# Kernel optimization log

Measured on AMD Instinct MI355X. Metric: run time of the kernel, lower is better.

Reference implementation:

```python
import jax, jax.numpy as jnp
import numpy as np

HIDDEN = 256
ATOM_DIM = 133
BOND_DIM = 14
MOL_DIM = 200
N_ATOMS = 120000
N_BONDS = 240000
MAX_DEG = 6
N_MOL = 4096
DEPTH = 3
EPS = 1e-5
NEG_SLOPE = 0.01


def _leaky(x):
    return jnp.where(x >= 0, x, NEG_SLOPE * x)


def _bn(x, w, b):
    # BatchNorm1d in training mode: batch mean / biased batch variance
    mu = jnp.mean(x, axis=0)
    var = jnp.var(x, axis=0)
    return (x - mu) * jax.lax.rsqrt(var + EPS) * w + b


def setup_inputs() -> dict:
    key = jax.random.key(0)
    ks = jax.random.split(key, 12)
    s = 0.02
    return {
        "atom_features": jax.random.normal(ks[0], (N_ATOMS, ATOM_DIM), jnp.float32),
        "bond_features": jax.random.normal(ks[1], (N_BONDS, BOND_DIM), jnp.float32),
        "bond_index": jax.random.randint(ks[2], (2, N_BONDS), 0, N_ATOMS, jnp.int32),
        "molecule_features": jax.random.normal(ks[3], (N_MOL, MOL_DIM), jnp.float32),
        # 1-based bond ids; 0 means padding (maps to prepended zero row)
        "atom_incoming_bond_map": jax.random.randint(ks[4], (N_ATOMS, MAX_DEG), 0, N_BONDS + 1, jnp.int32),
        "bond_reverse_map": jax.random.randint(ks[5], (N_BONDS,), 0, N_BONDS, jnp.int32),
        "atom_to_mol": jnp.sort(jax.random.randint(ks[6], (N_ATOMS,), 0, N_MOL, jnp.int32)),
        "W_i_w": jax.random.normal(ks[7], (HIDDEN, ATOM_DIM + BOND_DIM), jnp.float32) * s,
        "W_i_b": jnp.zeros((HIDDEN,), jnp.float32),
        "W_m_w": jax.random.normal(ks[8], (HIDDEN, HIDDEN), jnp.float32) * s,
        "W_m_b": jnp.zeros((HIDDEN,), jnp.float32),
        "W_a_w": jax.random.normal(ks[9], (HIDDEN, ATOM_DIM + HIDDEN), jnp.float32) * s,
        "W_a_b": jnp.zeros((HIDDEN,), jnp.float32),
        "bn_w": jnp.ones((HIDDEN,), jnp.float32),
        "bn_b": jnp.zeros((HIDDEN,), jnp.float32),
    }


def _atom_incoming_sum(h, aibm):
    # padded_h[0] is the zero row; aibm holds 1-based bond indices (0 = pad)
    padded_h = jnp.concatenate([jnp.zeros((1, h.shape[1]), h.dtype), h], axis=0)
    return padded_h[aibm].sum(axis=1)  # [n_atoms, H]


def reference(atom_features, bond_features, bond_index, molecule_features,
              atom_incoming_bond_map, bond_reverse_map, atom_to_mol,
              W_i_w, W_i_b, W_m_w, W_m_b, W_a_w, W_a_b, bn_w, bn_b):
    src = bond_index[0]
    # initial bond hidden states
    x = jnp.concatenate([bond_features, atom_features[src]], axis=1)
    h0 = _bn(_leaky(x @ W_i_w.T + W_i_b), bn_w, bn_b)
    h = h0
    for _ in range(DEPTH):
        atom_sums = _atom_incoming_sum(h, atom_incoming_bond_map)
        # message for bond b (v->w): sum of incoming bonds at v minus reverse bond
        m = atom_sums[src] - h[bond_reverse_map]
        h = _bn(_leaky(h0 + m @ W_m_w.T + W_m_b), bn_w, bn_b)
        # dropout_prob = 0.0 -> identity
    # bond -> atom pooling (empty atoms yield the cached zero vector)
    m_v = _atom_incoming_sum(h, atom_incoming_bond_map)
    h_v = _bn(_leaky(jnp.concatenate([atom_features, m_v], axis=1) @ W_a_w.T + W_a_b), bn_w, bn_b)
    # atom -> molecule pooling
    h_mol = jax.ops.segment_sum(h_v, atom_to_mol, num_segments=molecule_features.shape[0])
    return jnp.concatenate([h_mol, molecule_features], axis=1)
```

## Files before the change

### kernel.cpp

```cpp
#include <hip/hip_runtime.h>
#include <hip/hip_bf16.h>
#include <stdint.h>

#define NBONDS 240000
#define NATOMS 120000
#define HID    256
#define ADIM   133
#define BDIM   14
#define MOLDIM 200
#define NMOL   4096
#define KI     160
#define KM     256
#define KA     416
#define OUTW   456
#define BN_EPS 1e-5f
#define SLOPE  0.01f

typedef unsigned short u16;
typedef unsigned int   u32;
typedef __attribute__((ext_vector_type(8))) short short8;
typedef __attribute__((ext_vector_type(4))) float f32x4;

__device__ __forceinline__ float bf2f(u16 b){
  u32 u = ((u32)b) << 16;
  return __builtin_bit_cast(float, u);
}
__device__ __forceinline__ u16 f2bf(float f){
  u32 u = __builtin_bit_cast(u32, f);
  u32 r = (u + 0x7FFFu + ((u >> 16) & 1u)) >> 16;
  return (u16)r;
}
__device__ __forceinline__ void gload16(const void* g, void* l){
  __builtin_amdgcn_global_load_lds((const __attribute__((address_space(1))) u32*)g,
                                   (__attribute__((address_space(3))) u32*)l, 16, 0, 0);
}
__device__ __forceinline__ float leaky(float v){ return v >= 0.f ? v : SLOPE*v; }

__global__ void zero_f(float* p, int n){
  int i = blockIdx.x*blockDim.x + threadIdx.x;
  if(i < n) p[i] = 0.f;
}
__global__ void diag_k(float* out, int n, float wsz){
  int i = blockIdx.x*blockDim.x + threadIdx.x;
  for(; i < n; i += gridDim.x*blockDim.x) out[i] = (i == 0) ? wsz : 0.f;
}

__global__ void cvt_weights(const float* wi, const float* wm, const float* wa,
                            u16* wib, u16* wmb, u16* wab){
  int idx = blockIdx.x*blockDim.x + threadIdx.x;
  const int T0 = 256*KI, T1 = T0 + 256*KM, T2 = T1 + 256*KA;
  for(; idx < T2; idx += gridDim.x*blockDim.x){
    if(idx < T0){
      int n = idx / KI, k = idx % KI;
      float v = 0.f;
      if(k < 133)      v = wi[n*147 + 14 + k];
      else if(k < 147) v = wi[n*147 + (k - 133)];
      wib[idx] = f2bf(v);
    } else if(idx < T1){
      int j = idx - T0;
      wmb[j] = f2bf(wm[j]);
    } else {
      int j = idx - T1;
      int n = j / KA, k = j % KA;
      float v = 0.f;
      if(k < 256)      v = wa[n*389 + 133 + k];
      else if(k < 389) v = wa[n*389 + (k - 256)];
      wab[j] = f2bf(v);
    }
  }
}

__global__ void affine_k(const float* __restrict__ stats, float* __restrict__ aff,
                         float invN, const float* __restrict__ bnw, const float* __restrict__ bnb){
  int c = threadIdx.x;
  float mu  = stats[c] * invN;
  float var = stats[256+c]*invN - mu*mu;
  float rs  = rsqrtf(var + BN_EPS);
  float sc  = rs * bnw[c];
  aff[c]     = sc;
  aff[256+c] = bnb[c] - mu*sc;
}

__global__ __launch_bounds__(256) void msg_k(
    const int* __restrict__ bidx, const int* __restrict__ brm,
    const int* __restrict__ aibm, const u16* __restrict__ Hin,
    const u16* __restrict__ zrow, const float* __restrict__ ain,
    u16* __restrict__ Mout)
{
  int t = threadIdx.x;
  int b = blockIdx.x*8 + (t>>5);
  int lane = t & 31;
  int src = bidx[b];
  int rev = brm[b];
  const u16* gb[7];
  int cnt = 0;
  #pragma unroll
  for(int j=0;j<6;j++){
    int id = aibm[src*6+j];
    gb[j] = (id>0) ? (Hin + (size_t)(id-1)*HID) : zrow;
    cnt += (id>0);
  }
  gb[6] = Hin + (size_t)rev*HID;
  int c = lane*8;
  short8 v[7];
  #pragma unroll
  for(int j=0;j<7;j++) v[j] = *(const short8*)(gb[j]+c);
  float cm1 = (float)(cnt-1);
  short8 o;
  #pragma unroll
  for(int e=0;e<8;e++){
    float s = 0.f;
    #pragma unroll
    for(int j=0;j<6;j++) s += bf2f((u16)v[j][e]);
    s -= bf2f((u16)v[6][e]);
    o[e] = (short)f2bf(ain[c+e]*s + cm1*ain[256+c+e]);
  }
  *(short8*)(Mout + (size_t)b*HID + c) = o;
}

__global__ __launch_bounds__(256) void msgv_k(
    const int* __restrict__ aibm, const u16* __restrict__ Hin,
    const u16* __restrict__ zrow, const float* __restrict__ ain,
    u16* __restrict__ Mv)
{
  int t = threadIdx.x;
  int a = blockIdx.x*8 + (t>>5);
  int lane = t & 31;
  const u16* gb[6];
  int cnt = 0;
  #pragma unroll
  for(int j=0;j<6;j++){
    int id = aibm[a*6+j];
    gb[j] = (id>0) ? (Hin + (size_t)(id-1)*HID) : zrow;
    cnt += (id>0);
  }
  int c = lane*8;
  short8 v[6];
  #pragma unroll
  for(int j=0;j<6;j++) v[j] = *(const short8*)(gb[j]+c);
  float cf = (float)cnt;
  short8 o;
  #pragma unroll
  for(int e=0;e<8;e++){
    float s = 0.f;
    #pragma unroll
    for(int j=0;j<6;j++) s += bf2f((u16)v[j][e]);
    o[e] = (short)f2bf(ain[c+e]*s + cf*ain[256+c+e]);
  }
  *(short8*)(Mv + (size_t)a*HID + c) = o;
}


__global__ __launch_bounds__(256) void gemm0_k(
    const float* __restrict__ bondf, const float* __restrict__ atomf,
    const int* __restrict__ bidx, const u16* __restrict__ wib,
    const float* __restrict__ bi_, u16* __restrict__ Hout,
    float* __restrict__ stats)
{
  __shared__ u16 lA[2][4][64][8];
  __shared__ u16 lB[2][4][256][8];
  __shared__ float sred[512];
  const int tid=threadIdx.x, wave=tid>>6, lane=tid&63;
  const int wm=wave>>1, wn=wave&1, l15=lane&15, l4=lane>>4;
  const int r=tid&63, c=tid>>6;
  const int row0=blockIdx.x*64, row=row0+r;
  const int src = bidx[row];

  f32x4 acc[2][8];
  #pragma unroll
  for(int i=0;i<2;i++)
    #pragma unroll
    for(int j=0;j<8;j++){ f32x4 z={0.f,0.f,0.f,0.f}; acc[i][j]=z; }

  auto stgB=[&](int buf,int ks){
    #pragma unroll
    for(int kc=0;kc<4;kc++)
      gload16(wib + (size_t)(wave*64+lane)*KI + ks*32 + kc*8, &lB[buf][kc][wave*64][0]);
  };
  auto stgA=[&](int buf,int ks){
    int k0 = ks*32 + c*8;
    short8 o;
    #pragma unroll
    for(int e=0;e<8;e++){
      int kg=k0+e; float x=0.f;
      if(kg<ADIM) x=atomf[(size_t)src*ADIM+kg];
      else if(kg<ADIM+BDIM) x=bondf[(size_t)row*BDIM+kg-ADIM];
      o[e]=(short)f2bf(x);
    }
    *(short8*)&lA[buf][c][r][0]=o;
  };
  auto mm=[&](int cur){
    short8 af[2];
    #pragma unroll
    for(int mf=0;mf<2;mf++) af[mf]=*(const short8*)&lA[cur][l4][wm*32+mf*16+l15][0];
    #pragma unroll
    for(int nf=0;nf<8;nf++){
      short8 b8=*(const short8*)&lB[cur][l4][wn*128+nf*16+l15][0];
      #pragma unroll
      for(int mf=0;mf<2;mf++)
        acc[mf][nf]=__builtin_amdgcn_mfma_f32_16x16x32_bf16(af[mf],b8,acc[mf][nf],0,0,0);
    }
  };

  stgA(0,0); stgB(0,0);
  __syncthreads();
  #pragma unroll
  for(int ks=0;ks<5;ks++){
    int cur=ks&1;
    if(ks<4){ stgA(cur^1,ks+1); stgB(cur^1,ks+1); }
    mm(cur);
    __syncthreads();
  }
  sred[tid]=0.f; sred[256+tid]=0.f;
  __syncthreads();
  #pragma unroll
  for(int nf=0;nf<8;nf++){
    int col=wn*128+nf*16+l15;
    float bc=bi_[col], ps=0.f, pq=0.f;
    #pragma unroll
    for(int mf=0;mf<2;mf++)
      #pragma unroll
      for(int j=0;j<4;j++){
        int grow=row0+wm*32+mf*16+l4*4+j;
        float h=leaky(acc[mf][nf][j]+bc);
        Hout[(size_t)grow*HID+col]=f2bf(h);
        ps+=h; pq+=h*h;
      }
    atomicAdd(&sred[col],ps); atomicAdd(&sred[256+col],pq);
  }
  __syncthreads();
  atomicAdd(&stats[tid],sred[tid]); atomicAdd(&stats[256+tid],sred[256+tid]);
}

__global__ __launch_bounds__(256) void gemml_k(
    const float* __restrict__ bondf, const float* __restrict__ atomf,
    const int* __restrict__ bidx, u16* __restrict__ Mh,
    const u16* __restrict__ wmb, const float* __restrict__ bm_,
    const u16* __restrict__ wib, const float* __restrict__ bi_,
    const float* __restrict__ aff0, float* __restrict__ stats)
{
  __shared__ u16 lA[2][4][64][8];
  __shared__ u16 lB[2][4][256][8];
  __shared__ float sred[512];
  const int tid=threadIdx.x, wave=tid>>6, lane=tid&63;
  const int wm=wave>>1, wn=wave&1, l15=lane&15, l4=lane>>4;
  const int r=tid&63, c=tid>>6;
  const int row0=blockIdx.x*64, row=row0+r;
  const int src = bidx[row];

  f32x4 acc[2][8];
  #pragma unroll
  for(int i=0;i<2;i++)
    #pragma unroll
    for(int j=0;j<8;j++){ f32x4 z={0.f,0.f,0.f,0.f}; acc[i][j]=z; }

  auto stgB=[&](int buf,int ks,const u16* W,int ldk){
    #pragma unroll
    for(int kc=0;kc<4;kc++)
      gload16(W + (size_t)(wave*64+lane)*ldk + ks*32 + kc*8, &lB[buf][kc][wave*64][0]);
  };
  auto stgA1=[&](int buf,int ks){
    gload16(Mh + (size_t)(row0+lane)*KM + ks*32 + wave*8, &lA[buf][wave][0][0]);
  };
  auto stgA0=[&](int buf,int ks){
    int k0 = ks*32 + c*8;
    short8 o;
    #pragma unroll
    for(int e=0;e<8;e++){
      int kg=k0+e; float x=0.f;
      if(kg<ADIM) x=atomf[(size_t)src*ADIM+kg];
      else if(kg<ADIM+BDIM) x=bondf[(size_t)row*BDIM+kg-ADIM];
      o[e]=(short)f2bf(x);
    }
    *(short8*)&lA[buf][c][r][0]=o;
  };
  auto mm=[&](int cur){
    short8 af[2];
    #pragma unroll
    for(int mf=0;mf<2;mf++) af[mf]=*(const short8*)&lA[cur][l4][wm*32+mf*16+l15][0];
    #pragma unroll
    for(int nf=0;nf<8;nf++){
      short8 b8=*(const short8*)&lB[cur][l4][wn*128+nf*16+l15][0];
      #pragma unroll
      for(int mf=0;mf<2;mf++)
        acc[mf][nf]=__builtin_amdgcn_mfma_f32_16x16x32_bf16(af[mf],b8,acc[mf][nf],0,0,0);
    }
  };

  stgA1(0,0); stgB(0,0,wmb,KM);
  __syncthreads();
  #pragma unroll
  for(int ks=0;ks<8;ks++){
    int cur=ks&1;
    if(ks<7){ stgA1(cur^1,ks+1); stgB(cur^1,ks+1,wmb,KM); }
    mm(cur);
    __syncthreads();
  }
  u32 p1[2][8][2];
  #pragma unroll
  for(int mf=0;mf<2;mf++)
    #pragma unroll
    for(int nf=0;nf<8;nf++){
      p1[mf][nf][0]=((u32)f2bf(acc[mf][nf][1])<<16)|f2bf(acc[mf][nf][0]);
      p1[mf][nf][1]=((u32)f2bf(acc[mf][nf][3])<<16)|f2bf(acc[mf][nf][2]);
      f32x4 z={0.f,0.f,0.f,0.f}; acc[mf][nf]=z;
    }

  stgA0(0,0); stgB(0,0,wib,KI);
  __syncthreads();
  #pragma unroll
  for(int ks=0;ks<5;ks++){
    int cur=ks&1;
    if(ks<4){ stgA0(cur^1,ks+1); stgB(cur^1,ks+1,wib,KI); }
    mm(cur);
    __syncthreads();
  }

  sred[tid]=0.f; sred[256+tid]=0.f;
  __syncthreads();
  #pragma unroll
  for(int nf=0;nf<8;nf++){
    int col=wn*128+nf*16+l15;
    float bic=bi_[col], bmc=bm_[col];
    float s0=aff0[col], t0=aff0[256+col];
    float ps=0.f,pq=0.f;
    #pragma unroll
    for(int mf=0;mf<2;mf++)
      #pragma unroll
      for(int j=0;j<4;j++){
        int grow=row0+wm*32+mf*16+l4*4+j;
        float v0 = leaky(acc[mf][nf][j]+bic);
        v0 = s0*v0 + t0;
        u32 pw = p1[mf][nf][j>>1];
        float u1 = bf2f((u16)((j&1) ? (pw>>16) : (pw&0xffff)));
        float h = leaky(v0 + u1 + bmc);
        Mh[(size_t)grow*HID+col]=f2bf(h);
        ps+=h; pq+=h*h;
      }
    atomicAdd(&sred[col],ps); atomicAdd(&sred[256+col],pq);
  }
  __syncthreads();
  atomicAdd(&stats[tid],sred[tid]); atomicAdd(&stats[256+tid],sred[256+tid]);
}

__global__ __launch_bounds__(256) void gemmf_k(
    const float* __restrict__ atomf, u16* __restrict__ Mv,
    const u16* __restrict__ wab, const float* __restrict__ ba_,
    float* __restrict__ stats)
{
  __shared__ u16 lA[2][4][64][8];
  __shared__ u16 lB[2][4][256][8];
  __shared__ float sred[512];
  const int tid=threadIdx.x, wave=tid>>6, lane=tid&63;
  const int wm=wave>>1, wn=wave&1, l15=lane&15, l4=lane>>4;
  const int r=tid&63, c=tid>>6;
  const int row0=blockIdx.x*64, row=row0+r;

  f32x4 acc[2][8];
  #pragma unroll
  for(int i=0;i<2;i++)
    #pragma unroll
    for(int j=0;j<8;j++){ f32x4 z={0.f,0.f,0.f,0.f}; acc[i][j]=z; }

  auto stgB=[&](int buf,int ks){
    #pragma unroll
    for(int kc=0;kc<4;kc++)
      gload16(wab + (size_t)(wave*64+lane)*KA + ks*32 + kc*8, &lB[buf][kc][wave*64][0]);
  };
  auto stgA=[&](int buf,int ks){
    if(ks<8){
      gload16(Mv + (size_t)(row0+lane)*KM + ks*32 + wave*8, &lA[buf][wave][0][0]);
    } else {
      int k0 = ks*32 + c*8 - 256;
      short8 o;
      #pragma unroll
      for(int e=0;e<8;e++){
        int kg = k0 + e;
        float x = (kg < ADIM) ? atomf[(size_t)row*ADIM + kg] : 0.f;
        o[e]=(short)f2bf(x);
      }
      *(short8*)&lA[buf][c][r][0]=o;
    }
  };
  auto mm=[&](int cur){
    short8 af[2];
    #pragma unroll
    for(int mf=0;mf<2;mf++) af[mf]=*(const short8*)&lA[cur][l4][wm*32+mf*16+l15][0];
    #pragma unroll
    for(int nf=0;nf<8;nf++){
      short8 b8=*(const short8*)&lB[cur][l4][wn*128+nf*16+l15][0];
      #pragma unroll
      for(int mf=0;mf<2;mf++)
        acc[mf][nf]=__builtin_amdgcn_mfma_f32_16x16x32_bf16(af[mf],b8,acc[mf][nf],0,0,0);
    }
  };

  stgA(0,0); stgB(0,0);
  __syncthreads();
  #pragma unroll
  for(int ks=0;ks<13;ks++){
    int cur=ks&1;
    if(ks<12){ stgA(cur^1,ks+1); stgB(cur^1,ks+1); }
    mm(cur);
    __syncthreads();
  }
  sred[tid]=0.f; sred[256+tid]=0.f;
  __syncthreads();
  #pragma unroll
  for(int nf=0;nf<8;nf++){
    int col=wn*128+nf*16+l15;
    float bc=ba_[col], ps=0.f,pq=0.f;
    #pragma unroll
    for(int mf=0;mf<2;mf++)
      #pragma unroll
      for(int j=0;j<4;j++){
        int grow=row0+wm*32+mf*16+l4*4+j;
        float h=leaky(acc[mf][nf][j]+bc);
        Mv[(size_t)grow*HID+col]=f2bf(h);
        ps+=h; pq+=h*h;
      }
    atomicAdd(&sred[col],ps); atomicAdd(&sred[256+col],pq);
  }
  __syncthreads();
  atomicAdd(&stats[tid],sred[tid]); atomicAdd(&stats[256+tid],sred[256+tid]);
}

__device__ __forceinline__ int lbound(const int* a, int n, int v){
  int lo = 0, hi = n;
  while(lo < hi){ int mid = (lo+hi) >> 1; if(a[mid] < v) lo = mid+1; else hi = mid; }
  return lo;
}

__global__ void pool_k(const u16* __restrict__ hv, const float* __restrict__ aff,
                       const int* __restrict__ a2m, const float* __restrict__ molf,
                       float* __restrict__ outp){
  int m = blockIdx.x;
  int t = threadIdx.x;
  int start = lbound(a2m, NATOMS, m);
  int end   = lbound(a2m, NATOMS, m+1);
  int rg = t >> 5, cg = t & 31;
  float s[8];
  #pragma unroll
  for(int j=0;j<8;j++) s[j] = 0.f;
  for(int a = start + rg; a < end; a += 8){
    short8 v = *(const short8*)(hv + (size_t)a*HID + cg*8);
    #pragma unroll
    for(int j=0;j<8;j++) s[j] += bf2f((u16)v[j]);
  }
  __shared__ float red[8][256];
  #pragma unroll
  for(int j=0;j<8;j++) red[rg][cg*8+j] = s[j];
  __syncthreads();
  if(t < 256){
    float S = 0.f;
    #pragma unroll
    for(int r=0;r<8;r++) S += red[r][t];
    float cnt = (float)(end - start);
    outp[(size_t)m*OUTW + t] = aff[t]*S + cnt*aff[256+t];
  }
  if(t < MOLDIM){
    outp[(size_t)m*OUTW + HID + t] = molf[(size_t)m*MOLDIM + t];
  }
}

extern "C" void kernel_launch(void* const* d_in, const int* in_sizes, int n_in,
                              void* d_out, int out_size, void* d_ws, size_t ws_size,
                              hipStream_t stream){
  const float* atomf = (const float*)d_in[0];
  const float* bondf = (const float*)d_in[1];
  const int*   bidx  = (const int*)  d_in[2];
  const float* molf  = (const float*)d_in[3];
  const int*   aibm  = (const int*)  d_in[4];
  const int*   brm   = (const int*)  d_in[5];
  const int*   a2m   = (const int*)  d_in[6];
  const float* wi    = (const float*)d_in[7];
  const float* bi    = (const float*)d_in[8];
  const float* wm    = (const float*)d_in[9];
  const float* bm    = (const float*)d_in[10];
  const float* wa    = (const float*)d_in[11];
  const float* ba    = (const float*)d_in[12];
  const float* bnw   = (const float*)d_in[13];
  const float* bnb   = (const float*)d_in[14];
  float* outp = (float*)d_out;

  char* wsp = (char*)d_ws;
  size_t off = 0;
  auto alloc = [&](size_t bytes)->void*{
    void* p = wsp + off; off += (bytes + 255) & ~(size_t)255; return p;
  };
  u16* HA   = (u16*)alloc((size_t)NBONDS*HID*2);
  u16* HB   = (u16*)alloc((size_t)NBONDS*HID*2);
  u16* wib  = (u16*)alloc((size_t)256*KI*2);
  u16* wmb  = (u16*)alloc((size_t)256*KM*2);
  u16* wab  = (u16*)alloc((size_t)256*KA*2);
  float* stats = (float*)alloc(5*512*sizeof(float));
  float* affn  = (float*)alloc(5*512*sizeof(float));
  float* zrowf = (float*)alloc(512);
  size_t need = off;

  if(ws_size < need){
    diag_k<<<1024, 256, 0, stream>>>(outp, out_size, (float)ws_size);
    return;
  }
  const u16* zrow = (const u16*)zrowf;

  zero_f<<<(5248+255)/256, 256, 0, stream>>>(stats, 5248);
  cvt_weights<<<416, 256, 0, stream>>>(wi, wm, wa, wib, wmb, wab);

  gemm0_k<<<NBONDS/64, 256, 0, stream>>>(bondf, atomf, bidx, wib, bi, HA, stats);
  affine_k<<<1, 256, 0, stream>>>(stats, affn, 1.f/NBONDS, bnw, bnb);

  for(int t=0; t<3; t++){
    const u16* Hin = (t & 1) ? HB : HA;
    u16*       Hm  = (t & 1) ? HA : HB;
    msg_k<<<NBONDS/8, 256, 0, stream>>>(bidx, brm, aibm, Hin, zrow,
                                        affn + t*512, Hm);
    gemml_k<<<NBONDS/64, 256, 0, stream>>>(bondf, atomf, bidx, Hm,
                                           wmb, bm, wib, bi, affn,
                                           stats + (t+1)*512);
    affine_k<<<1, 256, 0, stream>>>(stats + (t+1)*512, affn + (t+1)*512,
                                    1.f/NBONDS, bnw, bnb);
  }

  msgv_k<<<NATOMS/8, 256, 0, stream>>>(aibm, HB, zrow, affn + 3*512, HA);
  gemmf_k<<<NATOMS/64, 256, 0, stream>>>(atomf, HA, wab, ba, stats + 4*512);
  affine_k<<<1, 256, 0, stream>>>(stats + 4*512, affn + 4*512, 1.f/NATOMS, bnw, bnb);

  pool_k<<<NMOL, 256, 0, stream>>>(HA, affn + 4*512, a2m, molf, outp);
}
```

Measured before the change: 1.870 ms.

## Split GEMM output columns across two blocks and write to separate buffer

The three GEMM kernels now tile the 256 output columns into two 128-column halves via blockIdx.y. This halves accumulator registers and LDS per block and adds launch_bounds occupancy hints. gemml_k computes the W_i recompute first and folds its result into the accumulators, which removes the packed bf16 intermediate. Output now goes to a separate buffer instead of overwriting the input in place, so the ping-pong is fixed to HA/HB. In exchange, the A-operand gathers (atom features, messages) are loaded twice, once per column half.

Result: slower. 1.978 ms (+5.8%).

```diff
diff --git a/kernel.cpp b/kernel.cpp
--- a/kernel.cpp
+++ b/kernel.cpp
@@ -151,31 +151,36 @@
 }
 
 
-__global__ __launch_bounds__(256) void gemm0_k(
+__global__ __launch_bounds__(256,4) void gemm0_k(
     const float* __restrict__ bondf, const float* __restrict__ atomf,
     const int* __restrict__ bidx, const u16* __restrict__ wib,
     const float* __restrict__ bi_, u16* __restrict__ Hout,
     float* __restrict__ stats)
 {
   __shared__ u16 lA[2][4][64][8];
-  __shared__ u16 lB[2][4][256][8];
-  __shared__ float sred[512];
+  __shared__ u16 lB[2][4][128][8];
+  __shared__ float sred[256];
   const int tid=threadIdx.x, wave=tid>>6, lane=tid&63;
   const int wm=wave>>1, wn=wave&1, l15=lane&15, l4=lane>>4;
   const int r=tid&63, c=tid>>6;
   const int row0=blockIdx.x*64, row=row0+r;
+  const int coffs=blockIdx.y*128;
   const int src = bidx[row];
-
-  f32x4 acc[2][8];
+  const u16* W = wib + (size_t)coffs*KI;
+
+  f32x4 acc[2][4];
   #pragma unroll
   for(int i=0;i<2;i++)
     #pragma unroll
-    for(int j=0;j<8;j++){ f32x4 z={0.f,0.f,0.f,0.f}; acc[i][j]=z; }
+    for(int j=0;j<4;j++){ f32x4 z={0.f,0.f,0.f,0.f}; acc[i][j]=z; }
 
   auto stgB=[&](int buf,int ks){
     #pragma unroll
-    for(int kc=0;kc<4;kc++)
-      gload16(wib + (size_t)(wave*64+lane)*KI + ks*32 + kc*8, &lB[buf][kc][wave*64][0]);
+    for(int cc=0;cc<2;cc++){
+      int bi2 = cc*256 + wave*64;
+      int kc = bi2>>7, r0 = bi2&127;
+      gload16(W + (size_t)(r0+lane)*KI + ks*32 + kc*8, &lB[buf][kc][r0][0]);
+    }
   };
   auto stgA=[&](int buf,int ks){
     int k0 = ks*32 + c*8;
@@ -194,8 +199,8 @@
     #pragma unroll
     for(int mf=0;mf<2;mf++) af[mf]=*(const short8*)&lA[cur][l4][wm*32+mf*16+l15][0];
     #pragma unroll
-    for(int nf=0;nf<8;nf++){
-      short8 b8=*(const short8*)&lB[cur][l4][wn*128+nf*16+l15][0];
+    for(int nf=0;nf<4;nf++){
+      short8 b8=*(const short8*)&lB[cur][l4][wn*64+nf*16+l15][0];
       #pragma unroll
       for(int mf=0;mf<2;mf++)
         acc[mf][nf]=__builtin_amdgcn_mfma_f32_16x16x32_bf16(af[mf],b8,acc[mf][nf],0,0,0);
@@ -211,53 +216,64 @@
     mm(cur);
     __syncthreads();
   }
-  sred[tid]=0.f; sred[256+tid]=0.f;
-  __syncthreads();
-  #pragma unroll
-  for(int nf=0;nf<8;nf++){
-    int col=wn*128+nf*16+l15;
-    float bc=bi_[col], ps=0.f, pq=0.f;
+  sred[tid] = 0.f;
+  __syncthreads();
+  #pragma unroll
+  for(int nf=0;nf<4;nf++){
+    int s = wn*64+nf*16+l15;
+    int colg = coffs + s;
+    float bc=bi_[colg], ps=0.f, pq=0.f;
     #pragma unroll
     for(int mf=0;mf<2;mf++)
       #pragma unroll
       for(int j=0;j<4;j++){
         int grow=row0+wm*32+mf*16+l4*4+j;
         float h=leaky(acc[mf][nf][j]+bc);
-        Hout[(size_t)grow*HID+col]=f2bf(h);
+        Hout[(size_t)grow*HID+colg]=f2bf(h);
         ps+=h; pq+=h*h;
       }
-    atomicAdd(&sred[col],ps); atomicAdd(&sred[256+col],pq);
-  }
-  __syncthreads();
-  atomicAdd(&stats[tid],sred[tid]); atomicAdd(&stats[256+tid],sred[256+tid]);
-}
-
-__global__ __launch_bounds__(256) void gemml_k(
+    atomicAdd(&sred[s],ps); atomicAdd(&sred[128+s],pq);
+  }
+  __syncthreads();
+  if(tid<128){
+    atomicAdd(&stats[coffs+tid],     sred[tid]);
+    atomicAdd(&stats[256+coffs+tid], sred[128+tid]);
+  }
+}
+
+__global__ __launch_bounds__(256,4) void gemml_k(
     const float* __restrict__ bondf, const float* __restrict__ atomf,
-    const int* __restrict__ bidx, u16* __restrict__ Mh,
+    const int* __restrict__ bidx, const u16* __restrict__ Mh,
     const u16* __restrict__ wmb, const float* __restrict__ bm_,
     const u16* __restrict__ wib, const float* __restrict__ bi_,
-    const float* __restrict__ aff0, float* __restrict__ stats)
+    const float* __restrict__ aff0, u16* __restrict__ Hout,
+    float* __restrict__ stats)
 {
   __shared__ u16 lA[2][4][64][8];
-  __shared__ u16 lB[2][4][256][8];
-  __shared__ float sred[512];
+  __shared__ u16 lB[2][4][128][8];
+  __shared__ float sred[256];
   const int tid=threadIdx.x, wave=tid>>6, lane=tid&63;
   const int wm=wave>>1, wn=wave&1, l15=lane&15, l4=lane>>4;
   const int r=tid&63, c=tid>>6;
   const int row0=blockIdx.x*64, row=row0+r;
+  const int coffs=blockIdx.y*128;
   const int src = bidx[row];
-
-  f32x4 acc[2][8];
+  const u16* Wi = wib + (size_t)coffs*KI;
+  const u16* Wm = wmb + (size_t)coffs*KM;
+
+  f32x4 acc[2][4];
   #pragma unroll
   for(int i=0;i<2;i++)
     #pragma unroll
-    for(int j=0;j<8;j++){ f32x4 z={0.f,0.f,0.f,0.f}; acc[i][j]=z; }
+    for(int j=0;j<4;j++){ f32x4 z={0.f,0.f,0.f,0.f}; acc[i][j]=z; }
 
   auto stgB=[&](int buf,int ks,const u16* W,int ldk){
     #pragma unroll
-    for(int kc=0;kc<4;kc++)
-      gload16(W + (size_t)(wave*64+lane)*ldk + ks*32 + kc*8, &lB[buf][kc][wave*64][0]);
+    for(int cc=0;cc<2;cc++){
+      int bi2 = cc*256 + wave*64;
+      int kc = bi2>>7, r0 = bi2&127;
+      gload16(W + (size_t)(r0+lane)*ldk + ks*32 + kc*8, &lB[buf][kc][r0][0]);
+    }
   };
   auto stgA1=[&](int buf,int ks){
     gload16(Mh + (size_t)(row0+lane)*KM + ks*32 + wave*8, &lA[buf][wave][0][0]);
@@ -279,93 +295,100 @@
     #pragma unroll
     for(int mf=0;mf<2;mf++) af[mf]=*(const short8*)&lA[cur][l4][wm*32+mf*16+l15][0];
     #pragma unroll
-    for(int nf=0;nf<8;nf++){
-      short8 b8=*(const short8*)&lB[cur][l4][wn*128+nf*16+l15][0];
+    for(int nf=0;nf<4;nf++){
+      short8 b8=*(const short8*)&lB[cur][l4][wn*64+nf*16+l15][0];
       #pragma unroll
       for(int mf=0;mf<2;mf++)
         acc[mf][nf]=__builtin_amdgcn_mfma_f32_16x16x32_bf16(af[mf],b8,acc[mf][nf],0,0,0);
     }
   };
 
-  stgA1(0,0); stgB(0,0,wmb,KM);
+  stgA0(0,0); stgB(0,0,Wi,KI);
+  __syncthreads();
+  #pragma unroll
+  for(int ks=0;ks<5;ks++){
+    int cur=ks&1;
+    if(ks<4){ stgA0(cur^1,ks+1); stgB(cur^1,ks+1,Wi,KI); }
+    mm(cur);
+    __syncthreads();
+  }
+
+  #pragma unroll
+  for(int nf=0;nf<4;nf++){
+    int colg = coffs + wn*64+nf*16+l15;
+    float bic=bi_[colg], s0=aff0[colg], t0=aff0[256+colg], bmc=bm_[colg];
+    #pragma unroll
+    for(int mf=0;mf<2;mf++)
+      #pragma unroll
+      for(int j=0;j<4;j++){
+        float v = leaky(acc[mf][nf][j]+bic);
+        acc[mf][nf][j] = s0*v + t0 + bmc;
+      }
+  }
+
+  stgA1(0,0); stgB(0,0,Wm,KM);
   __syncthreads();
   #pragma unroll
   for(int ks=0;ks<8;ks++){
     int cur=ks&1;
-    if(ks<7){ stgA1(cur^1,ks+1); stgB(cur^1,ks+1,wmb,KM); }
+    if(ks<7){ stgA1(cur^1,ks+1); stgB(cur^1,ks+1,Wm,KM); }
     mm(cur);
     __syncthreads();
   }
-  u32 p1[2][8][2];
-  #pragma unroll
-  for(int mf=0;mf<2;mf++)
-    #pragma unroll
-    for(int nf=0;nf<8;nf++){
-      p1[mf][nf][0]=((u32)f2bf(acc[mf][nf][1])<<16)|f2bf(acc[mf][nf][0]);
-      p1[mf][nf][1]=((u32)f2bf(acc[mf][nf][3])<<16)|f2bf(acc[mf][nf][2]);
-      f32x4 z={0.f,0.f,0.f,0.f}; acc[mf][nf]=z;
-    }
-
-  stgA0(0,0); stgB(0,0,wib,KI);
-  __syncthreads();
-  #pragma unroll
-  for(int ks=0;ks<5;ks++){
-    int cur=ks&1;
-    if(ks<4){ stgA0(cur^1,ks+1); stgB(cur^1,ks+1,wib,KI); }
-    mm(cur);
-    __syncthreads();
-  }
-
-  sred[tid]=0.f; sred[256+tid]=0.f;
-  __syncthreads();
-  #pragma unroll
-  for(int nf=0;nf<8;nf++){
-    int col=wn*128+nf*16+l15;
-    float bic=bi_[col], bmc=bm_[col];
-    float s0=aff0[col], t0=aff0[256+col];
+
+  sred[tid] = 0.f;
+  __syncthreads();
+  #pragma unroll
+  for(int nf=0;nf<4;nf++){
+    int s = wn*64+nf*16+l15;
+    int colg = coffs + s;
     float ps=0.f,pq=0.f;
     #pragma unroll
     for(int mf=0;mf<2;mf++)
       #pragma unroll
       for(int j=0;j<4;j++){
         int grow=row0+wm*32+mf*16+l4*4+j;
-        float v0 = leaky(acc[mf][nf][j]+bic);
-        v0 = s0*v0 + t0;
-        u32 pw = p1[mf][nf][j>>1];
-        float u1 = bf2f((u16)((j&1) ? (pw>>16) : (pw&0xffff)));
-        float h = leaky(v0 + u1 + bmc);
-        Mh[(size_t)grow*HID+col]=f2bf(h);
+        float h = leaky(acc[mf][nf][j]);
+        Hout[(size_t)grow*HID+colg]=f2bf(h);
         ps+=h; pq+=h*h;
       }
-    atomicAdd(&sred[col],ps); atomicAdd(&sred[256+col],pq);
-  }
-  __syncthreads();
-  atomicAdd(&stats[tid],sred[tid]); atomicAdd(&stats[256+tid],sred[256+tid]);
-}
-
-__global__ __launch_bounds__(256) void gemmf_k(
-    const float* __restrict__ atomf, u16* __restrict__ Mv,
+    atomicAdd(&sred[s],ps); atomicAdd(&sred[128+s],pq);
+  }
+  __syncthreads();
+  if(tid<128){
+    atomicAdd(&stats[coffs+tid],     sred[tid]);
+    atomicAdd(&stats[256+coffs+tid], sred[128+tid]);
+  }
+}
+
+__global__ __launch_bounds__(256,4) void gemmf_k(
+    const float* __restrict__ atomf, const u16* __restrict__ Mv,
     const u16* __restrict__ wab, const float* __restrict__ ba_,
-    float* __restrict__ stats)
+    u16* __restrict__ Hvout, float* __restrict__ stats)
 {
   __shared__ u16 lA[2][4][64][8];
-  __shared__ u16 lB[2][4][256][8];
-  __shared__ float sred[512];
+  __shared__ u16 lB[2][4][128][8];
+  __shared__ float sred[256];
   const int tid=threadIdx.x, wave=tid>>6, lane=tid&63;
   const int wm=wave>>1, wn=wave&1, l15=lane&15, l4=lane>>4;
   const int r=tid&63, c=tid>>6;
   const int row0=blockIdx.x*64, row=row0+r;
-
-  f32x4 acc[2][8];
+  const int coffs=blockIdx.y*128;
+  const u16* W = wab + (size_t)coffs*KA;
+
+  f32x4 acc[2][4];
   #pragma unroll
   for(int i=0;i<2;i++)
     #pragma unroll
-    for(int j=0;j<8;j++){ f32x4 z={0.f,0.f,0.f,0.f}; acc[i][j]=z; }
+    for(int j=0;j<4;j++){ f32x4 z={0.f,0.f,0.f,0.f}; acc[i][j]=z; }
 
   auto stgB=[&](int buf,int ks){
     #pragma unroll
-    for(int kc=0;kc<4;kc++)
-      gload16(wab + (size_t)(wave*64+lane)*KA + ks*32 + kc*8, &lB[buf][kc][wave*64][0]);
+    for(int cc=0;cc<2;cc++){
+      int bi2 = cc*256 + wave*64;
+      int kc = bi2>>7, r0 = bi2&127;
+      gload16(W + (size_t)(r0+lane)*KA + ks*32 + kc*8, &lB[buf][kc][r0][0]);
+    }
   };
   auto stgA=[&](int buf,int ks){
     if(ks<8){
@@ -387,8 +410,8 @@
     #pragma unroll
     for(int mf=0;mf<2;mf++) af[mf]=*(const short8*)&lA[cur][l4][wm*32+mf*16+l15][0];
     #pragma unroll
-    for(int nf=0;nf<8;nf++){
-      short8 b8=*(const short8*)&lB[cur][l4][wn*128+nf*16+l15][0];
+    for(int nf=0;nf<4;nf++){
+      short8 b8=*(const short8*)&lB[cur][l4][wn*64+nf*16+l15][0];
       #pragma unroll
       for(int mf=0;mf<2;mf++)
         acc[mf][nf]=__builtin_amdgcn_mfma_f32_16x16x32_bf16(af[mf],b8,acc[mf][nf],0,0,0);
@@ -404,25 +427,29 @@
     mm(cur);
     __syncthreads();
   }
-  sred[tid]=0.f; sred[256+tid]=0.f;
-  __syncthreads();
-  #pragma unroll
-  for(int nf=0;nf<8;nf++){
-    int col=wn*128+nf*16+l15;
-    float bc=ba_[col], ps=0.f,pq=0.f;
+  sred[tid] = 0.f;
+  __syncthreads();
+  #pragma unroll
+  for(int nf=0;nf<4;nf++){
+    int s = wn*64+nf*16+l15;
+    int colg = coffs + s;
+    float bc=ba_[colg], ps=0.f,pq=0.f;
     #pragma unroll
     for(int mf=0;mf<2;mf++)
       #pragma unroll
       for(int j=0;j<4;j++){
         int grow=row0+wm*32+mf*16+l4*4+j;
         float h=leaky(acc[mf][nf][j]+bc);
-        Mv[(size_t)grow*HID+col]=f2bf(h);
+        Hvout[(size_t)grow*HID+colg]=f2bf(h);
         ps+=h; pq+=h*h;
       }
-    atomicAdd(&sred[col],ps); atomicAdd(&sred[256+col],pq);
-  }
-  __syncthreads();
-  atomicAdd(&stats[tid],sred[tid]); atomicAdd(&stats[256+tid],sred[256+tid]);
+    atomicAdd(&sred[s],ps); atomicAdd(&sred[128+s],pq);
+  }
+  __syncthreads();
+  if(tid<128){
+    atomicAdd(&stats[coffs+tid],     sred[tid]);
+    atomicAdd(&stats[256+coffs+tid], sred[128+tid]);
+  }
 }
 
 __device__ __forceinline__ int lbound(const int* a, int n, int v){
@@ -507,23 +534,21 @@
   zero_f<<<(5248+255)/256, 256, 0, stream>>>(stats, 5248);
   cvt_weights<<<416, 256, 0, stream>>>(wi, wm, wa, wib, wmb, wab);
 
-  gemm0_k<<<NBONDS/64, 256, 0, stream>>>(bondf, atomf, bidx, wib, bi, HA, stats);
+  gemm0_k<<<dim3(NBONDS/64,2), 256, 0, stream>>>(bondf, atomf, bidx, wib, bi, HA, stats);
   affine_k<<<1, 256, 0, stream>>>(stats, affn, 1.f/NBONDS, bnw, bnb);
 
   for(int t=0; t<3; t++){
-    const u16* Hin = (t & 1) ? HB : HA;
-    u16*       Hm  = (t & 1) ? HA : HB;
-    msg_k<<<NBONDS/8, 256, 0, stream>>>(bidx, brm, aibm, Hin, zrow,
-                                        affn + t*512, Hm);
-    gemml_k<<<NBONDS/64, 256, 0, stream>>>(bondf, atomf, bidx, Hm,
-                                           wmb, bm, wib, bi, affn,
-                                           stats + (t+1)*512);
+    msg_k<<<NBONDS/8, 256, 0, stream>>>(bidx, brm, aibm, HA, zrow,
+                                        affn + t*512, HB);
+    gemml_k<<<dim3(NBONDS/64,2), 256, 0, stream>>>(bondf, atomf, bidx, HB,
+                                                   wmb, bm, wib, bi, affn,
+                                                   HA, stats + (t+1)*512);
     affine_k<<<1, 256, 0, stream>>>(stats + (t+1)*512, affn + (t+1)*512,
                                     1.f/NBONDS, bnw, bnb);
   }
 
-  msgv_k<<<NATOMS/8, 256, 0, stream>>>(aibm, HB, zrow, affn + 3*512, HA);
-  gemmf_k<<<NATOMS/64, 256, 0, stream>>>(atomf, HA, wab, ba, stats + 4*512);
+  msgv_k<<<NATOMS/8, 256, 0, stream>>>(aibm, HA, zrow, affn + 3*512, HB);
+  gemmf_k<<<dim3(NATOMS/64,2), 256, 0, stream>>>(atomf, HB, wab, ba, HA, stats + 4*512);
   affine_k<<<1, 256, 0, stream>>>(stats + 4*512, affn + 4*512, 1.f/NATOMS, bnw, bnb);
 
   pool_k<<<NMOL, 256, 0, stream>>>(HA, affn + 4*512, a2m, molf, outp);
```
